# Kernel tuning notes

Measured on AMD Instinct MI355X. Metric: run time of the kernel, lower is better.

## Reference

```python
import jax, jax.numpy as jnp
import numpy as np

K, N = 1024, 16384


def setup_inputs() -> dict:
    key = jax.random.key(0)
    k1, k2 = jax.random.split(key)
    # event counts per location/time step (non-negative)
    obs = jax.random.randint(k1, (K, N), 0, 5).astype(jnp.float32)
    # excitation matrix, Uniform(0, 0.01) as in the torch init
    halpha = jax.random.uniform(k2, (K, K), dtype=jnp.float32) * 0.01
    # scalar decay parameter, init 2.0
    hbeta = jnp.array([2.0], dtype=jnp.float32)
    return {"obs": obs, "halpha": halpha, "hbeta": hbeta}


def reference(obs, halpha, hbeta):
    # obs: [K, N] event counts; halpha: [K, K]; hbeta: [1]
    K_, N_ = obs.shape
    hmu = obs.mean(axis=1) / 10.0 + 0.01          # [K]
    beta = hbeta[0]
    decay = jnp.exp(-beta)

    # S_t[k] = sum_{tp < t} beta * exp(-(t - tp) * beta) * obs[k, tp]
    # Exponential kernel admits exact recursion: S_{t+1} = e^{-beta} (S_t + beta * obs_t)
    def step(S, obs_t):
        return decay * (S + beta * obs_t), S

    _, S_all = jax.lax.scan(step, jnp.zeros((K_,), obs.dtype), obs.T)  # S_all: [N, K]

    # lam1[k, t] = sum_j halpha[k, j] * S_all[t, j]   (matches mm(halpha, Nt*kernel).sum(1))
    lam1 = jnp.einsum('kj,nj->kn', halpha, S_all)      # [K, N]
    lams = jax.nn.softplus(hmu[:, None] + lam1)        # [K, N]

    loglik = (obs * jnp.log(lams) - lams).sum()
    return loglik, lams
```

## Files before the change

kernel.cpp:

```cpp
#include <hip/hip_runtime.h>

#define KDIM 1024
#define NDIM 16384
#define CHUNKS 256
#define CLEN 64
#define KTILES 16

typedef __bf16 bf16_t;
typedef bf16_t bf16x8 __attribute__((ext_vector_type(8)));
typedef bf16_t bf16x4 __attribute__((ext_vector_type(4)));
typedef float f32x4 __attribute__((ext_vector_type(4)));

__device__ __forceinline__ void gload_lds16(const bf16_t* g, bf16_t* l) {
  __builtin_amdgcn_global_load_lds(
      (const __attribute__((address_space(1))) void*)g,
      (__attribute__((address_space(3))) void*)l, 16, 0, 0);
}

__global__ __launch_bounds__(256) void k_convert_alpha(const float* __restrict__ A,
                                                       bf16_t* __restrict__ Ab) {
  size_t i = ((size_t)blockIdx.x * 256 + threadIdx.x) * 4;
  float4 v = *reinterpret_cast<const float4*>(A + i);
  bf16x4 o;
  o[0] = (bf16_t)v.x; o[1] = (bf16_t)v.y; o[2] = (bf16_t)v.z; o[3] = (bf16_t)v.w;
  *reinterpret_cast<bf16x4*>(Ab + i) = o;
}

__global__ __launch_bounds__(256) void k_phase1(const float* __restrict__ obs,
                                                const float* __restrict__ hbeta,
                                                float* __restrict__ carry,
                                                float* __restrict__ psum) {
  int tid = blockIdx.x * 256 + threadIdx.x;
  int k = tid >> 8;
  int c = tid & (CHUNKS - 1);
  float beta = hbeta[0];
  float decay = expf(-beta);
  const float* p = obs + (size_t)k * NDIM + c * CLEN;
  float S = 0.f, sum = 0.f;
#pragma unroll
  for (int t = 0; t < CLEN; t += 4) {
    float4 v = *reinterpret_cast<const float4*>(p + t);
    S = decay * (S + beta * v.x);
    S = decay * (S + beta * v.y);
    S = decay * (S + beta * v.z);
    S = decay * (S + beta * v.w);
    sum += v.x + v.y + v.z + v.w;
  }
  carry[tid] = S;
  psum[tid] = sum;
}

__global__ __launch_bounds__(64) void k_phase2(const float* __restrict__ hbeta,
                                               float* __restrict__ carry,
                                               const float* __restrict__ psum,
                                               float* __restrict__ hmu) {
  int k = blockIdx.x * blockDim.x + threadIdx.x;
  if (k >= KDIM) return;
  float beta = hbeta[0];
  float dL = expf(-beta * (float)CLEN);
  float Cg = 0.f, tot = 0.f;
  float* pc = carry + (size_t)k * CHUNKS;
  const float* pp = psum + (size_t)k * CHUNKS;
  for (int c = 0; c < CHUNKS; ++c) {
    float loc = pc[c];
    pc[c] = Cg;
    Cg = dL * Cg + loc;
    tot += pp[c];
  }
  hmu[k] = tot * (1.0f / NDIM) * 0.1f + 0.01f;
}

__global__ __launch_bounds__(64) void k_phase3(const float* __restrict__ obs,
                                               const float* __restrict__ hbeta,
                                               const float* __restrict__ carry,
                                               bf16_t* __restrict__ S_all) {
  int c  = blockIdx.x & (CHUNKS - 1);
  int kb = blockIdx.x >> 8;
  int lane = threadIdx.x;
  float beta = hbeta[0];
  float decay = expf(-beta);
  __shared__ float  obs_s[64][65];
  __shared__ bf16_t out_s[64][72];
  int k0 = kb * 64, t0 = c * CLEN;
#pragma unroll 4
  for (int r = 0; r < 64; ++r)
    obs_s[r][lane] = obs[(size_t)(k0 + r) * NDIM + t0 + lane];
  __syncthreads();
  float S = carry[(size_t)(k0 + lane) * CHUNKS + c];
#pragma unroll 8
  for (int t = 0; t < CLEN; ++t) {
    out_s[t][lane] = (bf16_t)S;
    S = decay * (S + beta * obs_s[lane][t]);
  }
  __syncthreads();
#pragma unroll 4
  for (int t = 0; t < CLEN; ++t)
    S_all[(size_t)(t0 + t) * KDIM + k0 + lane] = out_s[t][lane];
}

__global__ __launch_bounds__(512, 2) void k_gemm(const bf16_t* __restrict__ Ab,
                                                 const bf16_t* __restrict__ Bb,
                                                 const float* __restrict__ hmu,
                                                 const float* __restrict__ obs,
                                                 float* __restrict__ out) {
  __shared__ bf16_t As[2][256 * 64];
  __shared__ bf16_t Bs[2][256 * 64];
  int tid = threadIdx.x;
  int b = blockIdx.x;
  int lb = (b & 7) * 32 + (b >> 3);
  int kb = lb & 3;
  int tb = lb >> 2;
  int lane = tid & 63, wid = tid >> 6;
  int wm = wid >> 2, wn = wid & 3;
  int r15 = lane & 15, h = lane >> 4;
  f32x4 acc[8][4] = {};

  const bf16_t* gA[4];
  const bf16_t* gB[4];
#pragma unroll
  for (int i = 0; i < 4; ++i) {
    int slot = i * 512 + tid;
    int row = slot >> 3, sp = slot & 7;
    int sl = sp ^ (row & 7);
    gA[i] = Ab + (size_t)(kb * 256 + row) * KDIM + sl * 8;
    gB[i] = Bb + (size_t)(tb * 256 + row) * KDIM + sl * 8;
  }

#define STAGE_A(buf, kkoff) do { \
  _Pragma("unroll") \
  for (int i = 0; i < 4; ++i) \
    gload_lds16(gA[i] + (kkoff), &As[buf][(i * 512 + wid * 64) * 8]); \
} while (0)
#define STAGE_B(buf, kkoff) do { \
  _Pragma("unroll") \
  for (int i = 0; i < 4; ++i) \
    gload_lds16(gB[i] + (kkoff), &Bs[buf][(i * 512 + wid * 64) * 8]); \
} while (0)

  STAGE_A(0, 0);
  STAGE_B(0, 0);
  asm volatile("s_waitcnt vmcnt(0)" ::: "memory");
  __builtin_amdgcn_s_barrier();

  int cur = 0;
  for (int kt = 0; kt < KTILES; ++kt) {
    bf16x8 bfr[4][2];
#pragma unroll
    for (int ph = 0; ph < 4; ++ph) {
      bf16x8 af[2][2];
      if (ph == 0) {
#pragma unroll
        for (int ni = 0; ni < 4; ++ni)
#pragma unroll
          for (int kh = 0; kh < 2; ++kh) {
            int row = wn * 64 + ni * 16 + r15;
            bfr[ni][kh] = *reinterpret_cast<const bf16x8*>(
                &Bs[cur][row * 64 + (((kh * 4 + h) ^ (row & 7)) * 8)]);
          }
      }
#pragma unroll
      for (int m2 = 0; m2 < 2; ++m2)
#pragma unroll
        for (int kh = 0; kh < 2; ++kh) {
          int row = wm * 128 + (ph * 2 + m2) * 16 + r15;
          af[m2][kh] = *reinterpret_cast<const bf16x8*>(
              &As[cur][row * 64 + (((kh * 4 + h) ^ (row & 7)) * 8)]);
        }
      if (kt < KTILES - 1) {
        if (ph == 0) STAGE_A(cur ^ 1, (kt + 1) * 64);
        if (ph == 1) STAGE_B(cur ^ 1, (kt + 1) * 64);
      }
      __builtin_amdgcn_s_barrier();
      __builtin_amdgcn_s_setprio(1);
#pragma unroll
      for (int m2 = 0; m2 < 2; ++m2)
#pragma unroll
        for (int ni = 0; ni < 4; ++ni)
#pragma unroll
          for (int kh = 0; kh < 2; ++kh)
            acc[ph * 2 + m2][ni] = __builtin_amdgcn_mfma_f32_16x16x32_bf16(
                af[m2][kh], bfr[ni][kh], acc[ph * 2 + m2][ni], 0, 0, 0);
      __builtin_amdgcn_s_setprio(0);
      if (ph == 3)
        asm volatile("s_waitcnt vmcnt(0)" ::: "memory");
      __builtin_amdgcn_s_barrier();
    }
    cur ^= 1;
  }
#undef STAGE_A
#undef STAGE_B

  float lsum = 0.f;
  float* lams = out + 1;
#pragma unroll
  for (int mi = 0; mi < 8; ++mi) {
    int krow0 = kb * 256 + wm * 128 + mi * 16 + h * 4;
#pragma unroll
    for (int ni = 0; ni < 4; ++ni) {
      int t = tb * 256 + wn * 64 + ni * 16 + r15;
#pragma unroll
      for (int r = 0; r < 4; ++r) {
        int krow = krow0 + r;
        float x = hmu[krow] + acc[mi][ni][r];
        float lam = fmaxf(x, 0.f) + __logf(1.f + __expf(-fabsf(x)));
        lams[(size_t)krow * NDIM + t] = lam;
        float o = obs[(size_t)krow * NDIM + t];
        lsum += o * __logf(lam) - lam;
      }
    }
  }
  lsum += __shfl_down(lsum, 32);
  lsum += __shfl_down(lsum, 16);
  lsum += __shfl_down(lsum, 8);
  lsum += __shfl_down(lsum, 4);
  lsum += __shfl_down(lsum, 2);
  lsum += __shfl_down(lsum, 1);
  __shared__ float wsum[8];
  if (lane == 0) wsum[wid] = lsum;
  __syncthreads();
  if (tid == 0) {
    float s = 0.f;
#pragma unroll
    for (int w = 0; w < 8; ++w) s += wsum[w];
    atomicAdd(out, s);
  }
}

extern "C" void kernel_launch(void* const* d_in, const int* in_sizes, int n_in,
                              void* d_out, int out_size, void* d_ws, size_t ws_size,
                              hipStream_t stream) {
  const float* obs    = (const float*)d_in[0];
  const float* halpha = (const float*)d_in[1];
  const float* hbeta  = (const float*)d_in[2];
  float* out = (float*)d_out;

  char* ws = (char*)d_ws;
  bf16_t* S_all = (bf16_t*)ws;
  float*  carry = (float*)(ws + (size_t)NDIM * KDIM * 2);
  float*  psum  = carry + (size_t)KDIM * CHUNKS;
  float*  hmu   = psum + (size_t)KDIM * CHUNKS;
  bf16_t* Ab    = (bf16_t*)(hmu + KDIM);

  hipMemsetAsync(d_out, 0, sizeof(float), stream);
  k_convert_alpha<<<(KDIM * KDIM) / (256 * 4), 256, 0, stream>>>(halpha, Ab);
  k_phase1<<<(KDIM * CHUNKS) / 256, 256, 0, stream>>>(obs, hbeta, carry, psum);
  k_phase2<<<16, 64, 0, stream>>>(hbeta, carry, psum, hmu);
  k_phase3<<<(KDIM / 64) * CHUNKS, 64, 0, stream>>>(obs, hbeta, carry, S_all);
  k_gemm<<<4 * (NDIM / 256), 512, 0, stream>>>(Ab, S_all, hmu, obs, out);
}
```

Baseline: 112.7 us.

## Restructure GEMM k-loop into k-half stages with two barriers per tile

Rewrites the bf16 MFMA main loop of the fused GEMM+softplus kernel. The four per-phase barrier pairs become one barrier pair per k-tile. The A prefetch is issued at the top of the tile with a partial vmcnt wait, and the B prefetch is issued mid-tile. Fragments are now loaded per k-half (A in two groups of four, B shared), which aims to cut synchronisation and give the scheduler longer MFMA runs. The cost is a different load/compute interleave that relies on the vmcnt accounting being right and could change register pressure.

After: 115.3 us. 2.4% more time.

```diff
diff --git a/kernel.cpp b/kernel.cpp
--- a/kernel.cpp
+++ b/kernel.cpp
@@ -137,58 +137,74 @@
     gload_lds16(gB[i] + (kkoff), &Bs[buf][(i * 512 + wid * 64) * 8]); \
 } while (0)
 
+#define A_FRAG(mi, sl) (*reinterpret_cast<const bf16x8*>( \
+    &As[cur][(wm * 128 + (mi) * 16 + r15) * 64 + ((((sl)) ^ ((wm * 128 + (mi) * 16 + r15) & 7)) * 8)]))
+#define B_FRAG(ni, sl) (*reinterpret_cast<const bf16x8*>( \
+    &Bs[cur][(wn * 64 + (ni) * 16 + r15) * 64 + ((((sl)) ^ ((wn * 64 + (ni) * 16 + r15) & 7)) * 8)]))
+
   STAGE_A(0, 0);
   STAGE_B(0, 0);
-  asm volatile("s_waitcnt vmcnt(0)" ::: "memory");
-  __builtin_amdgcn_s_barrier();
 
   int cur = 0;
   for (int kt = 0; kt < KTILES; ++kt) {
-    bf16x8 bfr[4][2];
-#pragma unroll
-    for (int ph = 0; ph < 4; ++ph) {
-      bf16x8 af[2][2];
-      if (ph == 0) {
-#pragma unroll
-        for (int ni = 0; ni < 4; ++ni)
-#pragma unroll
-          for (int kh = 0; kh < 2; ++kh) {
-            int row = wn * 64 + ni * 16 + r15;
-            bfr[ni][kh] = *reinterpret_cast<const bf16x8*>(
-                &Bs[cur][row * 64 + (((kh * 4 + h) ^ (row & 7)) * 8)]);
-          }
-      }
-#pragma unroll
-      for (int m2 = 0; m2 < 2; ++m2)
-#pragma unroll
-        for (int kh = 0; kh < 2; ++kh) {
-          int row = wm * 128 + (ph * 2 + m2) * 16 + r15;
-          af[m2][kh] = *reinterpret_cast<const bf16x8*>(
-              &As[cur][row * 64 + (((kh * 4 + h) ^ (row & 7)) * 8)]);
-        }
-      if (kt < KTILES - 1) {
-        if (ph == 0) STAGE_A(cur ^ 1, (kt + 1) * 64);
-        if (ph == 1) STAGE_B(cur ^ 1, (kt + 1) * 64);
-      }
-      __builtin_amdgcn_s_barrier();
-      __builtin_amdgcn_s_setprio(1);
-#pragma unroll
-      for (int m2 = 0; m2 < 2; ++m2)
-#pragma unroll
-        for (int ni = 0; ni < 4; ++ni)
-#pragma unroll
-          for (int kh = 0; kh < 2; ++kh)
-            acc[ph * 2 + m2][ni] = __builtin_amdgcn_mfma_f32_16x16x32_bf16(
-                af[m2][kh], bfr[ni][kh], acc[ph * 2 + m2][ni], 0, 0, 0);
-      __builtin_amdgcn_s_setprio(0);
-      if (ph == 3)
-        asm volatile("s_waitcnt vmcnt(0)" ::: "memory");
-      __builtin_amdgcn_s_barrier();
+    __builtin_amdgcn_sched_barrier(0);
+    __builtin_amdgcn_s_barrier();
+    if (kt < KTILES - 1) {
+      STAGE_A(cur ^ 1, (kt + 1) * 64);
+      asm volatile("s_waitcnt vmcnt(4)" ::: "memory");
+    } else {
+      asm volatile("s_waitcnt vmcnt(0)" ::: "memory");
     }
+    __builtin_amdgcn_s_barrier();
+
+    bf16x8 a0[4], a1[4], bf0[4];
+#pragma unroll
+    for (int m = 0; m < 4; ++m) a0[m] = A_FRAG(m, h);
+#pragma unroll
+    for (int n = 0; n < 4; ++n) bf0[n] = B_FRAG(n, h);
+    __builtin_amdgcn_s_setprio(1);
+#pragma unroll
+    for (int m = 0; m < 4; ++m)
+#pragma unroll
+      for (int n = 0; n < 4; ++n)
+        acc[m][n] = __builtin_amdgcn_mfma_f32_16x16x32_bf16(a0[m], bf0[n], acc[m][n], 0, 0, 0);
+    __builtin_amdgcn_s_setprio(0);
+#pragma unroll
+    for (int m = 0; m < 4; ++m) a1[m] = A_FRAG(4 + m, h);
+    __builtin_amdgcn_s_setprio(1);
+#pragma unroll
+    for (int m = 0; m < 4; ++m)
+#pragma unroll
+      for (int n = 0; n < 4; ++n)
+        acc[4 + m][n] = __builtin_amdgcn_mfma_f32_16x16x32_bf16(a1[m], bf0[n], acc[4 + m][n], 0, 0, 0);
+    __builtin_amdgcn_s_setprio(0);
+    if (kt < KTILES - 1) STAGE_B(cur ^ 1, (kt + 1) * 64);
+#pragma unroll
+    for (int m = 0; m < 4; ++m) a0[m] = A_FRAG(m, 4 + h);
+#pragma unroll
+    for (int n = 0; n < 4; ++n) bf0[n] = B_FRAG(n, 4 + h);
+    __builtin_amdgcn_s_setprio(1);
+#pragma unroll
+    for (int m = 0; m < 4; ++m)
+#pragma unroll
+      for (int n = 0; n < 4; ++n)
+        acc[m][n] = __builtin_amdgcn_mfma_f32_16x16x32_bf16(a0[m], bf0[n], acc[m][n], 0, 0, 0);
+    __builtin_amdgcn_s_setprio(0);
+#pragma unroll
+    for (int m = 0; m < 4; ++m) a1[m] = A_FRAG(4 + m, 4 + h);
+    __builtin_amdgcn_s_setprio(1);
+#pragma unroll
+    for (int m = 0; m < 4; ++m)
+#pragma unroll
+      for (int n = 0; n < 4; ++n)
+        acc[4 + m][n] = __builtin_amdgcn_mfma_f32_16x16x32_bf16(a1[m], bf0[n], acc[4 + m][n], 0, 0, 0);
+    __builtin_amdgcn_s_setprio(0);
     cur ^= 1;
   }
 #undef STAGE_A
 #undef STAGE_B
+#undef A_FRAG
+#undef B_FRAG
 
   float lsum = 0.f;
   float* lams = out + 1;
```
